# Kernel tuning notes

Hardware: AMD Instinct MI355X
Metric: run time of the kernel (lower is better)

## Reference

```python
import jax, jax.numpy as jnp
import numpy as np
from jax import lax

K2 = 3                 # support_kernel_size
TARGET_OCC = 0.5
OCC_W = 10.0
ITERS = 10             # flood-fill iterations
THRESH = 0.5
STEEP = 20.0

# 6-neighbor 3D cross kernel (plus-shaped), shape [O=1, I=1, 3, 3, 3]
_cross_np = np.zeros((1, 1, 3, 3, 3), dtype=np.float32)
for dz, dy, dx in [(0, 1, 1), (2, 1, 1), (1, 0, 1), (1, 2, 1), (1, 1, 0), (1, 1, 2)]:
    _cross_np[0, 0, dz, dy, dx] = 1.0


def _conv3d(x, k, pad):
    # x: [B, C, D, H, W], k: [O, I, kd, kh, kw]
    return lax.conv_general_dilated(
        x, k, window_strides=(1, 1, 1), padding=pad,
        dimension_numbers=('NCDHW', 'OIDHW', 'NCDHW'))


def setup_inputs() -> dict:
    key = jax.random.key(0)
    voxel_grid = jax.random.uniform(key, (4, 1, 128, 128, 128), dtype=jnp.float32)
    return {"voxel_grid": voxel_grid}


def reference(voxel_grid):
    B, C, D, H, W = voxel_grid.shape
    N = B * D * H * W
    dt = voxel_grid.dtype

    # ---- overhang score: vectorized over all z-slices at once ----
    # per-slice conv2d(3x3 ones) == conv3d with kernel depth 1
    k2 = jnp.ones((1, 1, 1, K2, K2), dt)
    below = voxel_grid[:, :, :-1]          # [B,1,D-1,H,W]
    curr = voxel_grid[:, :, 1:]
    below_support = _conv3d(below, k2, ((0, 0), (1, 1), (1, 1)))
    support_ratio = below_support / (K2 * K2)
    overhang = (curr * (1.0 - support_ratio)).sum() / N

    # ---- surface area score ----
    k3 = jnp.ones((1, 1, 3, 3, 3), dt)
    neighbor_solid = _conv3d(voxel_grid, k3, ((1, 1), (1, 1), (1, 1)))
    surface_term = neighbor_solid.sum() / 27.0 / N

    occupancy = voxel_grid.sum() / N
    occupancy_penalty = OCC_W * (occupancy - TARGET_OCC) ** 2

    # differentiable flood-fill (diff_find_enclosed_voids)
    seed = jnp.zeros_like(voxel_grid).at[:, :, 5, 5, 5].set(1.0)
    cross = jnp.asarray(_cross_np, dt)
    not_solid = 1.0 - voxel_grid

    def body(i, mask):
        c = _conv3d(mask, cross, ((1, 1), (1, 1), (1, 1)))
        act = jax.nn.sigmoid(STEEP * (c - THRESH))
        return jnp.maximum(mask, act) * not_solid

    enclosed = lax.fori_loop(0, ITERS, body, seed)
    resin_trap_penalty = 100.0 * enclosed.sum() / N

    surface_score = surface_term - resin_trap_penalty - occupancy_penalty
    return overhang, surface_score
```

## Files before the change

### kernel.cpp

```cpp
#include <hip/hip_runtime.h>

#define HW    (128*128)
#define DHW   (128*128*128)
#define NTOT  (4*DHW)
#define NBLK  (16*128*4)

__device__ __forceinline__ float sigf(float x){ return 1.0f/(1.0f+__expf(-x)); }
__device__ __forceinline__ float4 ld4(const float* p){ return *(const float4*)p; }


__global__ __launch_bounds__(256) void reduce_all_k(
    const float* __restrict__ v, float* __restrict__ p_occ,
    float* __restrict__ p_surf, float* __restrict__ p_over)
{
    __shared__ float rows[10][132];
    __shared__ float sm[3][4];

    const int tx = threadIdx.x, ty = threadIdx.y;
    const int tid = ty*32 + tx;
    const int y0 = blockIdx.x*8;
    const int y  = y0 + ty;
    const int z  = blockIdx.y;
    const int b  = blockIdx.z;
    const int x4 = tx*4;
    const size_t idx = (size_t)b*DHW + ((size_t)z*128 + y)*128 + x4;

    if (z >= 1) {
        const float* bp = v + (size_t)b*DHW + (size_t)(z-1)*HW;
        const float4 zero = make_float4(0,0,0,0);
        for (int i = tid; i < 320; i += 256) {
            int r = i >> 5, q = (i & 31)*4;
            int gy = y0 - 1 + r;
            float4 qv = ((unsigned)gy <= 127u) ? ld4(bp + (size_t)gy*128 + q) : zero;
            *(float4*)&rows[r][q] = qv;
        }
        if (tid < 20) rows[tid>>1][130 + (tid&1)] = 0.f;
    }
    __syncthreads();

    float4 val = ld4(v + idx);
    float occ = val.x + val.y + val.z + val.w;

    float wz = (z==0 || z==127) ? 2.f : 3.f;
    float wy = (y==0 || y==127) ? 2.f : 3.f;
    float wx0 = (x4==0)   ? 2.f : 3.f;
    float wx3 = (x4==124) ? 2.f : 3.f;
    float surf = wz*wy*(wx0*val.x + 3.f*val.y + 3.f*val.z + wx3*val.w);

    float over = 0.f;
    if (z >= 1) {
        float sx=0, sy=0, szz=0, sw=0;
        #pragma unroll
        for (int dy = 0; dy < 3; ++dy) {
            const float* R = rows[ty + dy];
            float4 q = *(const float4*)&R[x4];
            float ql = R[(tx==0)  ? 130 : x4-1];
            float qr = R[(tx==31) ? 131 : x4+4];
            sx  += ql  + q.x + q.y;
            sy  += q.x + q.y + q.z;
            szz += q.y + q.z + q.w;
            sw  += q.z + q.w + qr;
        }
        const float inv9 = 1.f/9.f;
        over = val.x*(1.f - sx*inv9) + val.y*(1.f - sy*inv9)
             + val.z*(1.f - szz*inv9) + val.w*(1.f - sw*inv9);
    }

    #pragma unroll
    for (int o = 32; o; o >>= 1) {
        occ  += __shfl_down(occ,  o, 64);
        surf += __shfl_down(surf, o, 64);
        over += __shfl_down(over, o, 64);
    }
    int lane = tid & 63, wid = tid >> 6;
    if (lane == 0) { sm[0][wid]=occ; sm[1][wid]=surf; sm[2][wid]=over; }
    __syncthreads();
    if (tid == 0) {
        int blin = (b*gridDim.y + blockIdx.y)*gridDim.x + blockIdx.x;
        p_occ [blin] = sm[0][0]+sm[0][1]+sm[0][2]+sm[0][3];
        p_surf[blin] = sm[1][0]+sm[1][1]+sm[1][2]+sm[1][3];
        p_over[blin] = sm[2][0]+sm[2][1]+sm[2][2]+sm[2][3];
    }
}

__global__ __launch_bounds__(256) void trap_box_k(
    const float* __restrict__ v, float* __restrict__ p_trap)
{
    __shared__ float mbuf[2][17][17][20];
    __shared__ float nvL[16][16][20];
    __shared__ float red[4];

    const int b = blockIdx.x;
    const size_t gb = (size_t)b * DHW;
    const int tid = threadIdx.x;
    const int ty = tid & 15, tz = tid >> 4;
    const float a_lo = sigf(-10.0f), a_hi = sigf(10.0f);
    const float4 zero4 = make_float4(0,0,0,0);

    float m[16];
    {
        const float* rv = v + gb + ((size_t)tz*128 + ty)*128;
        int dzy = abs(tz-5) + abs(ty-5);
        #pragma unroll
        for (int q = 0; q < 4; ++q) {
            int x4 = 4*q;
            float4 a = ld4(rv + x4);
            float nv0=1.f-a.x, nv1=1.f-a.y, nv2=1.f-a.z, nv3=1.f-a.w;
            *(float4*)&nvL[tz][ty][x4] = make_float4(nv0,nv1,nv2,nv3);
            int d0 = dzy+abs(x4+0-5), d1 = dzy+abs(x4+1-5);
            int d2 = dzy+abs(x4+2-5), d3 = dzy+abs(x4+3-5);
            m[x4+0] = ((d0==0)?1.f:((d0==1)?a_hi:a_lo)) * nv0;
            m[x4+1] = ((d1==0)?1.f:((d1==1)?a_hi:a_lo)) * nv1;
            m[x4+2] = ((d2==0)?1.f:((d2==1)?a_hi:a_lo)) * nv2;
            m[x4+3] = ((d3==0)?1.f:((d3==1)?a_hi:a_lo)) * nv3;
            *(float4*)&mbuf[0][tz][ty][x4] = make_float4(m[x4+0],m[x4+1],m[x4+2],m[x4+3]);
        }
    }
    {
        #pragma unroll
        for (int f = 0; f < 3; ++f) {
            int a = tid >> 4, e = tid & 15;
            int zz, yy, xx;
            if (f == 0)      { zz = 16; yy = a;  xx = e;  }
            else if (f == 1) { zz = a;  yy = 16; xx = e;  }
            else             { zz = a;  yy = e;  xx = 16; }
            float bgv = a_lo * (1.f - v[gb + ((size_t)zz*128 + yy)*128 + xx]);
            mbuf[0][zz][yy][xx] = bgv;
            mbuf[1][zz][yy][xx] = bgv;
        }
    }
    __syncthreads();

    int cur = 0;
    for (int it = 0; it < 9; ++it) {
        const float* YM = &mbuf[cur][tz][ty-1][0];
        const float* YP = &mbuf[cur][tz][ty+1][0];
        const float* ZM = &mbuf[cur][tz-1][ty][0];
        const float* ZP = &mbuf[cur][tz+1][ty][0];
        const float  xrE = mbuf[cur][tz][ty][16];
        float* W = &mbuf[cur^1][tz][ty][0];
        float nm[16];
        #pragma unroll
        for (int q = 0; q < 4; ++q) {
            int x4 = 4*q;
            float4 ym = (ty > 0) ? *(const float4*)&YM[x4] : zero4;
            float4 yp = *(const float4*)&YP[x4];
            float4 zm = (tz > 0) ? *(const float4*)&ZM[x4] : zero4;
            float4 zp = *(const float4*)&ZP[x4];
            float4 nv = *(const float4*)&nvL[tz][ty][x4];
            float xl = (q == 0) ? 0.f : m[x4-1];
            float xr = (q == 3) ? xrE : m[x4+4];
            float s0 = xl      + m[x4+1] + ym.x + yp.x + zm.x + zp.x;
            float s1 = m[x4+0] + m[x4+2] + ym.y + yp.y + zm.y + zp.y;
            float s2 = m[x4+1] + m[x4+3] + ym.z + yp.z + zm.z + zp.z;
            float s3 = m[x4+2] + xr      + ym.w + yp.w + zm.w + zp.w;
            nm[x4+0] = fmaxf(m[x4+0], sigf(20.f*s0 - 10.f)) * nv.x;
            nm[x4+1] = fmaxf(m[x4+1], sigf(20.f*s1 - 10.f)) * nv.y;
            nm[x4+2] = fmaxf(m[x4+2], sigf(20.f*s2 - 10.f)) * nv.z;
            nm[x4+3] = fmaxf(m[x4+3], sigf(20.f*s3 - 10.f)) * nv.w;
            *(float4*)&W[x4] = make_float4(nm[x4+0],nm[x4+1],nm[x4+2],nm[x4+3]);
        }
        #pragma unroll
        for (int x = 0; x < 16; ++x) m[x] = nm[x];
        __syncthreads();
        cur ^= 1;
    }

    float d = 0.f;
    #pragma unroll
    for (int x = 0; x < 16; ++x) d += m[x] - a_lo * nvL[tz][ty][x];
    #pragma unroll
    for (int o = 32; o; o >>= 1) d += __shfl_down(d, o, 64);
    int lane = tid & 63, wid = tid >> 6;
    if (lane == 0) red[wid] = d;
    __syncthreads();
    if (tid == 0) p_trap[b] = red[0] + red[1] + red[2] + red[3];
}

__global__ __launch_bounds__(1024) void finalize_k(
    const float* __restrict__ p_occ, const float* __restrict__ p_surf,
    const float* __restrict__ p_over, const float* __restrict__ p_trap,
    float* __restrict__ out)
{
    double occ=0, surf=0, over=0;
    for (int i = threadIdx.x; i < NBLK; i += 1024) {
        occ += p_occ[i]; surf += p_surf[i]; over += p_over[i];
    }
    __shared__ double sm[3][16];
    #pragma unroll
    for (int o = 32; o; o >>= 1) {
        occ  += __shfl_down(occ,  o, 64);
        surf += __shfl_down(surf, o, 64);
        over += __shfl_down(over, o, 64);
    }
    int lane = threadIdx.x & 63, wid = threadIdx.x >> 6;
    if (lane == 0) { sm[0][wid]=occ; sm[1][wid]=surf; sm[2][wid]=over; }
    __syncthreads();
    if (threadIdx.x == 0) {
        double so=0, ss=0, sv=0;
        for (int w = 0; w < 16; ++w) { so+=sm[0][w]; ss+=sm[1][w]; sv+=sm[2][w]; }
        double dS = (double)p_trap[0] + p_trap[1] + p_trap[2] + p_trap[3];
        double a_lo = 1.0 / (1.0 + exp(10.0));
        double N = (double)NTOT;
        double trap_sum = a_lo * (N - so) + dS;
        double occupancy = so / N;
        double occ_pen = 10.0 * (occupancy - 0.5) * (occupancy - 0.5);
        out[0] = (float)(sv / N);
        out[1] = (float)(ss / 27.0 / N - 100.0 * trap_sum / N - occ_pen);
    }
}

extern "C" void kernel_launch(void* const* d_in, const int* in_sizes, int n_in,
                              void* d_out, int out_size, void* d_ws, size_t ws_size,
                              hipStream_t stream)
{
    const float* v = (const float*)d_in[0];
    float* out = (float*)d_out;
    float* ws = (float*)d_ws;

    float* p_occ  = ws;
    float* p_surf = p_occ  + NBLK;
    float* p_over = p_surf + NBLK;
    float* p_trap = p_over + NBLK;

    reduce_all_k<<<dim3(16,128,4), dim3(32,8,1), 0, stream>>>(v, p_occ, p_surf, p_over);
    trap_box_k<<<4, 256, 0, stream>>>(v, p_trap);
    finalize_k<<<1, 1024, 0, stream>>>(p_occ, p_surf, p_over, p_trap, out);
}
```

Before: 100.5 us.

## Fuse trap flood-fill and reduction kernels into one heterogeneous launch

Merges the flood-fill box kernel and the per-slice reduction kernel into a single launch, where the first four blocks run the flood fill and the rest do the reductions. The slow 4-block flood fill now overlaps with the bulk reduction work instead of running serially after it. The flood fill drops its double buffer and the separate not-solid buffer in shared memory: it keeps not-solid values in registers and adds a second barrier per iteration. Shared memory is unioned so the reduction blocks can reach higher occupancy.

```diff
diff --git a/kernel.cpp b/kernel.cpp
--- a/kernel.cpp
+++ b/kernel.cpp
@@ -3,178 +3,172 @@
 #define HW    (128*128)
 #define DHW   (128*128*128)
 #define NTOT  (4*DHW)
-#define NBLK  (16*128*4)
+#define NBLK  8192
 
 __device__ __forceinline__ float sigf(float x){ return 1.0f/(1.0f+__expf(-x)); }
 __device__ __forceinline__ float4 ld4(const float* p){ return *(const float4*)p; }
 
 
-__global__ __launch_bounds__(256) void reduce_all_k(
+__global__ __launch_bounds__(256, 4) void mega_k(
     const float* __restrict__ v, float* __restrict__ p_occ,
-    float* __restrict__ p_surf, float* __restrict__ p_over)
+    float* __restrict__ p_surf, float* __restrict__ p_over,
+    float* __restrict__ p_trap)
 {
-    __shared__ float rows[10][132];
-    __shared__ float sm[3][4];
-
-    const int tx = threadIdx.x, ty = threadIdx.y;
-    const int tid = ty*32 + tx;
-    const int y0 = blockIdx.x*8;
-    const int y  = y0 + ty;
-    const int z  = blockIdx.y;
-    const int b  = blockIdx.z;
-    const int x4 = tx*4;
-    const size_t idx = (size_t)b*DHW + ((size_t)z*128 + y)*128 + x4;
-
-    if (z >= 1) {
-        const float* bp = v + (size_t)b*DHW + (size_t)(z-1)*HW;
-        const float4 zero = make_float4(0,0,0,0);
-        for (int i = tid; i < 320; i += 256) {
-            int r = i >> 5, q = (i & 31)*4;
-            int gy = y0 - 1 + r;
-            float4 qv = ((unsigned)gy <= 127u) ? ld4(bp + (size_t)gy*128 + q) : zero;
-            *(float4*)&rows[r][q] = qv;
-        }
-        if (tid < 20) rows[tid>>1][130 + (tid&1)] = 0.f;
-    }
-    __syncthreads();
-
-    float4 val = ld4(v + idx);
-    float occ = val.x + val.y + val.z + val.w;
-
-    float wz = (z==0 || z==127) ? 2.f : 3.f;
-    float wy = (y==0 || y==127) ? 2.f : 3.f;
-    float wx0 = (x4==0)   ? 2.f : 3.f;
-    float wx3 = (x4==124) ? 2.f : 3.f;
-    float surf = wz*wy*(wx0*val.x + 3.f*val.y + 3.f*val.z + wx3*val.w);
-
-    float over = 0.f;
-    if (z >= 1) {
-        float sx=0, sy=0, szz=0, sw=0;
+    __shared__ float4 smem4[1445];
+    __shared__ float sred[16];
+    float* smem = (float*)smem4;
+
+    const int bid = blockIdx.x;
+    const int tid = threadIdx.x;
+
+    if (bid < 4) {
+        const int b = bid;
+        const size_t gb = (size_t)b * DHW;
+        const int ty = tid & 15, tz = tid >> 4;
+        const float a_lo = sigf(-10.0f), a_hi = sigf(10.0f);
+        const float4 zero4 = make_float4(0,0,0,0);
+        #define M(zz,yy) (smem + (((zz)*17 + (yy))*20))
+
+        float m[16], nv[16];
+        {
+            const float* rv = v + gb + ((size_t)tz*128 + ty)*128;
+            int dzy = abs(tz-5) + abs(ty-5);
+            #pragma unroll
+            for (int q = 0; q < 4; ++q) {
+                int x4 = 4*q;
+                float4 a = ld4(rv + x4);
+                nv[x4+0]=1.f-a.x; nv[x4+1]=1.f-a.y; nv[x4+2]=1.f-a.z; nv[x4+3]=1.f-a.w;
+                int d0=dzy+abs(x4+0-5), d1=dzy+abs(x4+1-5);
+                int d2=dzy+abs(x4+2-5), d3=dzy+abs(x4+3-5);
+                m[x4+0] = ((d0==0)?1.f:((d0==1)?a_hi:a_lo)) * nv[x4+0];
+                m[x4+1] = ((d1==0)?1.f:((d1==1)?a_hi:a_lo)) * nv[x4+1];
+                m[x4+2] = ((d2==0)?1.f:((d2==1)?a_hi:a_lo)) * nv[x4+2];
+                m[x4+3] = ((d3==0)?1.f:((d3==1)?a_hi:a_lo)) * nv[x4+3];
+                *(float4*)(M(tz,ty) + x4) = make_float4(m[x4+0],m[x4+1],m[x4+2],m[x4+3]);
+            }
+        }
+        const float xrE = a_lo * (1.f - v[gb + ((size_t)tz*128 + ty)*128 + 16]);
+        {
+            int a = tid >> 4, e = tid & 15;
+            M(16,a)[e] = a_lo * (1.f - v[gb + ((size_t)16*128 + a)*128 + e]);
+            M(a,16)[e] = a_lo * (1.f - v[gb + ((size_t)a*128 + 16)*128 + e]);
+        }
+        __syncthreads();
+
+        for (int it = 0; it < 9; ++it) {
+            const float* YM = M(tz,ty-1);
+            const float* YP = M(tz,ty+1);
+            const float* ZM = M(tz-1,ty);
+            const float* ZP = M(tz+1,ty);
+            float nm[16];
+            #pragma unroll
+            for (int q = 0; q < 4; ++q) {
+                int x4 = 4*q;
+                float4 ym = (ty > 0) ? *(const float4*)(YM + x4) : zero4;
+                float4 yp = *(const float4*)(YP + x4);
+                float4 zm = (tz > 0) ? *(const float4*)(ZM + x4) : zero4;
+                float4 zp = *(const float4*)(ZP + x4);
+                float xl = (q == 0) ? 0.f : m[x4-1];
+                float xr = (q == 3) ? xrE : m[x4+4];
+                float s0 = xl      + m[x4+1] + ym.x + yp.x + zm.x + zp.x;
+                float s1 = m[x4+0] + m[x4+2] + ym.y + yp.y + zm.y + zp.y;
+                float s2 = m[x4+1] + m[x4+3] + ym.z + yp.z + zm.z + zp.z;
+                float s3 = m[x4+2] + xr      + ym.w + yp.w + zm.w + zp.w;
+                nm[x4+0] = fmaxf(m[x4+0], sigf(20.f*s0 - 10.f)) * nv[x4+0];
+                nm[x4+1] = fmaxf(m[x4+1], sigf(20.f*s1 - 10.f)) * nv[x4+1];
+                nm[x4+2] = fmaxf(m[x4+2], sigf(20.f*s2 - 10.f)) * nv[x4+2];
+                nm[x4+3] = fmaxf(m[x4+3], sigf(20.f*s3 - 10.f)) * nv[x4+3];
+            }
+            __syncthreads();
+            float* W = M(tz,ty);
+            #pragma unroll
+            for (int q = 0; q < 4; ++q) {
+                int x4 = 4*q;
+                *(float4*)(W + x4) = make_float4(nm[x4+0],nm[x4+1],nm[x4+2],nm[x4+3]);
+                m[x4+0]=nm[x4+0]; m[x4+1]=nm[x4+1]; m[x4+2]=nm[x4+2]; m[x4+3]=nm[x4+3];
+            }
+            __syncthreads();
+        }
+
+        float d = 0.f;
         #pragma unroll
-        for (int dy = 0; dy < 3; ++dy) {
-            const float* R = rows[ty + dy];
-            float4 q = *(const float4*)&R[x4];
-            float ql = R[(tx==0)  ? 130 : x4-1];
-            float qr = R[(tx==31) ? 131 : x4+4];
-            sx  += ql  + q.x + q.y;
-            sy  += q.x + q.y + q.z;
-            szz += q.y + q.z + q.w;
-            sw  += q.z + q.w + qr;
-        }
-        const float inv9 = 1.f/9.f;
-        over = val.x*(1.f - sx*inv9) + val.y*(1.f - sy*inv9)
-             + val.z*(1.f - szz*inv9) + val.w*(1.f - sw*inv9);
-    }
-
-    #pragma unroll
-    for (int o = 32; o; o >>= 1) {
-        occ  += __shfl_down(occ,  o, 64);
-        surf += __shfl_down(surf, o, 64);
-        over += __shfl_down(over, o, 64);
-    }
-    int lane = tid & 63, wid = tid >> 6;
-    if (lane == 0) { sm[0][wid]=occ; sm[1][wid]=surf; sm[2][wid]=over; }
-    __syncthreads();
-    if (tid == 0) {
-        int blin = (b*gridDim.y + blockIdx.y)*gridDim.x + blockIdx.x;
-        p_occ [blin] = sm[0][0]+sm[0][1]+sm[0][2]+sm[0][3];
-        p_surf[blin] = sm[1][0]+sm[1][1]+sm[1][2]+sm[1][3];
-        p_over[blin] = sm[2][0]+sm[2][1]+sm[2][2]+sm[2][3];
-    }
-}
-
-__global__ __launch_bounds__(256) void trap_box_k(
-    const float* __restrict__ v, float* __restrict__ p_trap)
-{
-    __shared__ float mbuf[2][17][17][20];
-    __shared__ float nvL[16][16][20];
-    __shared__ float red[4];
-
-    const int b = blockIdx.x;
-    const size_t gb = (size_t)b * DHW;
-    const int tid = threadIdx.x;
-    const int ty = tid & 15, tz = tid >> 4;
-    const float a_lo = sigf(-10.0f), a_hi = sigf(10.0f);
-    const float4 zero4 = make_float4(0,0,0,0);
-
-    float m[16];
-    {
-        const float* rv = v + gb + ((size_t)tz*128 + ty)*128;
-        int dzy = abs(tz-5) + abs(ty-5);
+        for (int x = 0; x < 16; ++x) d += m[x] - a_lo * nv[x];
         #pragma unroll
-        for (int q = 0; q < 4; ++q) {
-            int x4 = 4*q;
-            float4 a = ld4(rv + x4);
-            float nv0=1.f-a.x, nv1=1.f-a.y, nv2=1.f-a.z, nv3=1.f-a.w;
-            *(float4*)&nvL[tz][ty][x4] = make_float4(nv0,nv1,nv2,nv3);
-            int d0 = dzy+abs(x4+0-5), d1 = dzy+abs(x4+1-5);
-            int d2 = dzy+abs(x4+2-5), d3 = dzy+abs(x4+3-5);
-            m[x4+0] = ((d0==0)?1.f:((d0==1)?a_hi:a_lo)) * nv0;
-            m[x4+1] = ((d1==0)?1.f:((d1==1)?a_hi:a_lo)) * nv1;
-            m[x4+2] = ((d2==0)?1.f:((d2==1)?a_hi:a_lo)) * nv2;
-            m[x4+3] = ((d3==0)?1.f:((d3==1)?a_hi:a_lo)) * nv3;
-            *(float4*)&mbuf[0][tz][ty][x4] = make_float4(m[x4+0],m[x4+1],m[x4+2],m[x4+3]);
-        }
-    }
-    {
+        for (int o = 32; o; o >>= 1) d += __shfl_down(d, o, 64);
+        int lane = tid & 63, wid = tid >> 6;
+        if (lane == 0) sred[wid] = d;
+        __syncthreads();
+        if (tid == 0) p_trap[b] = sred[0] + sred[1] + sred[2] + sred[3];
+        #undef M
+    } else {
+        const int rid = bid - 4;
+        const int b   = rid >> 11;
+        const int rem = rid & 2047;
+        const int z   = rem >> 4;
+        const int y0  = (rem & 15) * 8;
+        const int tx  = tid & 31, ty = tid >> 5;
+        const int y   = y0 + ty;
+        const int x4  = tx * 4;
+        const size_t idx = (size_t)b*DHW + ((size_t)z*128 + y)*128 + x4;
+        #define ROWS(r) (smem + (r)*132)
+
+        if (z >= 1) {
+            const float* bp = v + (size_t)b*DHW + (size_t)(z-1)*HW;
+            const float4 zero = make_float4(0,0,0,0);
+            for (int i = tid; i < 320; i += 256) {
+                int r = i >> 5, q = (i & 31)*4;
+                int gy = y0 - 1 + r;
+                float4 qv = ((unsigned)gy <= 127u) ? ld4(bp + (size_t)gy*128 + q) : zero;
+                *(float4*)(ROWS(r) + q) = qv;
+            }
+            if (tid < 20) ROWS(tid>>1)[130 + (tid&1)] = 0.f;
+        }
+        __syncthreads();
+
+        float4 val = ld4(v + idx);
+        float occ = val.x + val.y + val.z + val.w;
+
+        float wz = (z==0 || z==127) ? 2.f : 3.f;
+        float wy = (y==0 || y==127) ? 2.f : 3.f;
+        float wx0 = (x4==0)   ? 2.f : 3.f;
+        float wx3 = (x4==124) ? 2.f : 3.f;
+        float surf = wz*wy*(wx0*val.x + 3.f*val.y + 3.f*val.z + wx3*val.w);
+
+        float over = 0.f;
+        if (z >= 1) {
+            float sx=0, sy=0, szz=0, sw=0;
+            #pragma unroll
+            for (int dy = 0; dy < 3; ++dy) {
+                const float* R = ROWS(ty + dy);
+                float4 q = *(const float4*)(R + x4);
+                float ql = R[(tx==0)  ? 130 : x4-1];
+                float qr = R[(tx==31) ? 131 : x4+4];
+                sx  += ql  + q.x + q.y;
+                sy  += q.x + q.y + q.z;
+                szz += q.y + q.z + q.w;
+                sw  += q.z + q.w + qr;
+            }
+            const float inv9 = 1.f/9.f;
+            over = val.x*(1.f - sx*inv9) + val.y*(1.f - sy*inv9)
+                 + val.z*(1.f - szz*inv9) + val.w*(1.f - sw*inv9);
+        }
+
         #pragma unroll
-        for (int f = 0; f < 3; ++f) {
-            int a = tid >> 4, e = tid & 15;
-            int zz, yy, xx;
-            if (f == 0)      { zz = 16; yy = a;  xx = e;  }
-            else if (f == 1) { zz = a;  yy = 16; xx = e;  }
-            else             { zz = a;  yy = e;  xx = 16; }
-            float bgv = a_lo * (1.f - v[gb + ((size_t)zz*128 + yy)*128 + xx]);
-            mbuf[0][zz][yy][xx] = bgv;
-            mbuf[1][zz][yy][xx] = bgv;
-        }
-    }
-    __syncthreads();
-
-    int cur = 0;
-    for (int it = 0; it < 9; ++it) {
-        const float* YM = &mbuf[cur][tz][ty-1][0];
-        const float* YP = &mbuf[cur][tz][ty+1][0];
-        const float* ZM = &mbuf[cur][tz-1][ty][0];
-        const float* ZP = &mbuf[cur][tz+1][ty][0];
-        const float  xrE = mbuf[cur][tz][ty][16];
-        float* W = &mbuf[cur^1][tz][ty][0];
-        float nm[16];
-        #pragma unroll
-        for (int q = 0; q < 4; ++q) {
-            int x4 = 4*q;
-            float4 ym = (ty > 0) ? *(const float4*)&YM[x4] : zero4;
-            float4 yp = *(const float4*)&YP[x4];
-            float4 zm = (tz > 0) ? *(const float4*)&ZM[x4] : zero4;
-            float4 zp = *(const float4*)&ZP[x4];
-            float4 nv = *(const float4*)&nvL[tz][ty][x4];
-            float xl = (q == 0) ? 0.f : m[x4-1];
-            float xr = (q == 3) ? xrE : m[x4+4];
-            float s0 = xl      + m[x4+1] + ym.x + yp.x + zm.x + zp.x;
-            float s1 = m[x4+0] + m[x4+2] + ym.y + yp.y + zm.y + zp.y;
-            float s2 = m[x4+1] + m[x4+3] + ym.z + yp.z + zm.z + zp.z;
-            float s3 = m[x4+2] + xr      + ym.w + yp.w + zm.w + zp.w;
-            nm[x4+0] = fmaxf(m[x4+0], sigf(20.f*s0 - 10.f)) * nv.x;
-            nm[x4+1] = fmaxf(m[x4+1], sigf(20.f*s1 - 10.f)) * nv.y;
-            nm[x4+2] = fmaxf(m[x4+2], sigf(20.f*s2 - 10.f)) * nv.z;
-            nm[x4+3] = fmaxf(m[x4+3], sigf(20.f*s3 - 10.f)) * nv.w;
-            *(float4*)&W[x4] = make_float4(nm[x4+0],nm[x4+1],nm[x4+2],nm[x4+3]);
-        }
-        #pragma unroll
-        for (int x = 0; x < 16; ++x) m[x] = nm[x];
-        __syncthreads();
-        cur ^= 1;
-    }
-
-    float d = 0.f;
-    #pragma unroll
-    for (int x = 0; x < 16; ++x) d += m[x] - a_lo * nvL[tz][ty][x];
-    #pragma unroll
-    for (int o = 32; o; o >>= 1) d += __shfl_down(d, o, 64);
-    int lane = tid & 63, wid = tid >> 6;
-    if (lane == 0) red[wid] = d;
-    __syncthreads();
-    if (tid == 0) p_trap[b] = red[0] + red[1] + red[2] + red[3];
+        for (int o = 32; o; o >>= 1) {
+            occ  += __shfl_down(occ,  o, 64);
+            surf += __shfl_down(surf, o, 64);
+            over += __shfl_down(over, o, 64);
+        }
+        int lane = tid & 63, wid = tid >> 6;
+        if (lane == 0) { sred[wid]=occ; sred[4+wid]=surf; sred[8+wid]=over; }
+        __syncthreads();
+        if (tid == 0) {
+            p_occ [rid] = sred[0]+sred[1]+sred[2]+sred[3];
+            p_surf[rid] = sred[4]+sred[5]+sred[6]+sred[7];
+            p_over[rid] = sred[8]+sred[9]+sred[10]+sred[11];
+        }
+        #undef ROWS
+    }
 }
 
 __global__ __launch_bounds__(1024) void finalize_k(
@@ -223,7 +217,6 @@
     float* p_over = p_surf + NBLK;
     float* p_trap = p_over + NBLK;
 
-    reduce_all_k<<<dim3(16,128,4), dim3(32,8,1), 0, stream>>>(v, p_occ, p_surf, p_over);
-    trap_box_k<<<4, 256, 0, stream>>>(v, p_trap);
+    mega_k<<<NBLK + 4, 256, 0, stream>>>(v, p_occ, p_surf, p_over, p_trap);
     finalize_k<<<1, 1024, 0, stream>>>(p_occ, p_surf, p_over, p_trap, out);
 }
```

Measured after the change: 89.23 us. 11.2% less time.
